# Kernel optimization log

Measured on AMD Instinct MI355X. Metric: run time of the kernel, lower is better.

The kernel has to match this reference:

```python
import jax, jax.numpy as jnp
import numpy as np

B, N, D, H, K = 8, 1024, 1024, 64, 20


def setup_inputs() -> dict:
    key = jax.random.key(0)
    ks = jax.random.split(key, 8)
    s = 0.05
    return {
        "f1": jax.random.normal(ks[0], (B, N, D), jnp.float32),
        "f2": jax.random.normal(ks[1], (B, N, D), jnp.float32),
        "W1a": jax.random.normal(ks[2], (D, H), jnp.float32) * s,
        "b1a": jnp.zeros((H,), jnp.float32),
        "W2a": jax.random.normal(ks[3], (H, H), jnp.float32) * s,
        "b2a": jnp.zeros((H,), jnp.float32),
        "W1b": jax.random.normal(ks[4], (H, H), jnp.float32) * s,
        "b1b": jnp.zeros((H,), jnp.float32),
        "W2b": jax.random.normal(ks[5], (H, H), jnp.float32) * s,
        "b2b": jnp.zeros((H,), jnp.float32),
        "k": K,
    }


def _knn_idx(f, k):
    # f: [N, D] -> indices [N, k] of k nearest neighbors (self excluded)
    sq = jnp.sum(f * f, axis=-1)                      # [N]
    d = sq[:, None] + sq[None, :] - 2.0 * (f @ f.T)   # [N, N] squared dists
    n = f.shape[0]
    d = d + jnp.eye(n, dtype=f.dtype) * jnp.float32(1e10)  # exclude self-loop
    _, idx = jax.lax.top_k(-d, k)                     # smallest distances
    return idx


def _gin_layer(x, idx, W1, b1, W2, b2):
    # GINConv with eps=0: MLP(x + sum_{j in N(i)} x_j)
    agg = jnp.sum(x[idx], axis=1)                     # [N, D] neighbor-sum
    h = x + agg
    h = jnp.maximum(h @ W1 + b1, 0.0) @ W2 + b2
    return h


def reference(f1, f2, W1a, b1a, W2a, b2a, W1b, b1b, W2b, b2b, k):
    def encode(f):
        idx = _knn_idx(f, k)
        h = _gin_layer(f, idx, W1a, b1a, W2a, b2a)
        h = _gin_layer(h, idx, W1b, b1b, W2b, b2b)
        return h

    def per_sample(a, b):
        z1 = encode(a)                                # [N, H]
        z2 = encode(b)                                # [N, H]
        sim = z1 @ z2.T                               # [N, N]
        return jax.nn.softmax(sim, axis=1)

    return jax.vmap(per_sample)(f1, f2)               # [B, N, N]
```

## Files before the change

### kernel.cpp

```cpp
#include <hip/hip_runtime.h>
#include <hip/hip_bf16.h>
#include <math.h>

#define BATCH 8
#define NPTS  1024
#define DIM   1024
#define HID   64
#define KNN   20
#define NMAT  16
#define KPACK 3072

typedef __attribute__((ext_vector_type(8))) short short8;
typedef __attribute__((ext_vector_type(4))) float floatx4;

__device__ __forceinline__ const float* mat_base(const float* f1, const float* f2, int m) {
    return (m < BATCH) ? (f1 + (size_t)m * NPTS * DIM)
                       : (f2 + (size_t)(m - BATCH) * NPTS * DIM);
}

__device__ __forceinline__ unsigned short f2bf_bits(float v) {
    __hip_bfloat16 h = __float2bfloat16(v);
    return *(unsigned short*)&h;
}
__device__ __forceinline__ float bfbits2f(unsigned short b) {
    union { unsigned u; float f; } c; c.u = ((unsigned)b) << 16; return c.f;
}

__global__ __launch_bounds__(256) void split_ymlp_kernel(const float* __restrict__ f1,
                                                         const float* __restrict__ f2,
                                                         const float* __restrict__ W,
                                                         unsigned short* __restrict__ H,
                                                         float* __restrict__ sq,
                                                         float* __restrict__ y) {
    int row0 = blockIdx.x * 64;
    int m = row0 >> 10;
    const float* A = mat_base(f1, f2, m) + (size_t)(row0 & (NPTS - 1)) * DIM;
    unsigned short* Hb = H + (size_t)row0 * KPACK;
    __shared__ float As[64][20];
    __shared__ float Ws[16][HID];
    int tid = threadIdx.x;
    int r = tid >> 2, cq = (tid & 3) * 4;
    int ty = tid >> 4, tx = tid & 15;
    float acc[4][4];
    #pragma unroll
    for (int i = 0; i < 4; ++i)
        #pragma unroll
        for (int j = 0; j < 4; ++j) acc[i][j] = 0.f;
    float sqp = 0.f;
    unsigned short* Hr = Hb + (size_t)r * KPACK + cq;

    for (int kk = 0; kk < DIM; kk += 16) {
        float4 a = *(const float4*)&A[(size_t)r * DIM + kk + cq];
        {
            float vv[4] = {a.x, a.y, a.z, a.w};
            unsigned short h1[4], h2[4], h3[4];
            #pragma unroll
            for (int c = 0; c < 4; ++c) {
                unsigned short b1 = f2bf_bits(vv[c]);
                float r1 = vv[c] - bfbits2f(b1);
                unsigned short b2 = f2bf_bits(r1);
                float r2 = r1 - bfbits2f(b2);
                unsigned short b3 = f2bf_bits(r2);
                h1[c] = b1; h2[c] = b2; h3[c] = b3;
            }
            *(ushort4*)&Hr[kk]        = *(ushort4*)&h1[0];
            *(ushort4*)&Hr[1024 + kk] = *(ushort4*)&h2[0];
            *(ushort4*)&Hr[2048 + kk] = *(ushort4*)&h3[0];
            sqp += a.x * a.x + a.y * a.y + a.z * a.z + a.w * a.w;
        }
        *(float4*)&As[r][cq] = a;
        {
            int d = tid >> 4, hh = (tid & 15) * 4;
            *(float4*)&Ws[d][hh] = *(const float4*)&W[(size_t)(kk + d) * HID + hh];
        }
        __syncthreads();
        #pragma unroll
        for (int k = 0; k < 16; ++k) {
            float av[4];
            #pragma unroll
            for (int ii = 0; ii < 4; ++ii) av[ii] = As[ty * 4 + ii][k];
            float4 w = *(const float4*)&Ws[k][tx * 4];
            #pragma unroll
            for (int ii = 0; ii < 4; ++ii) {
                acc[ii][0] += av[ii] * w.x;
                acc[ii][1] += av[ii] * w.y;
                acc[ii][2] += av[ii] * w.z;
                acc[ii][3] += av[ii] * w.w;
            }
        }
        __syncthreads();
    }
    sqp += __shfl_down(sqp, 1);
    sqp += __shfl_down(sqp, 2);
    if ((tid & 3) == 0) sq[row0 + r] = sqp;
    #pragma unroll
    for (int ii = 0; ii < 4; ++ii)
        *(float4*)&y[(size_t)(row0 + ty * 4 + ii) * HID + tx * 4] = *(float4*)&acc[ii][0];
}

__global__ __launch_bounds__(256) void gram_mfma_kernel(const unsigned short* __restrict__ H,
                                                        const float* __restrict__ sq,
                                                        float* __restrict__ dist) {
    int bid = blockIdx.x;
    int xcd = bid & 7;
    int g = bid >> 3;
    int m = xcd + 8 * (g & 1);
    int t = g >> 1;
    int bi = 0;
    { int a = t; while (a >= 8 - bi) { a -= 8 - bi; ++bi; } t = a; }
    int bj = bi + t;
    int ti = bi << 7, tj = bj << 7;

    const unsigned short* Hm = H + (size_t)m * NPTS * KPACK;

    __shared__ __align__(16) unsigned short Asl[24 * 512];
    __shared__ __align__(16) unsigned short Bsl[24 * 512];

    int tid = threadIdx.x;
    int w = tid >> 6, lane = tid & 63;
    int wi = w >> 1, wj = w & 1;
    int r16 = lane & 15, kc = lane >> 4;

    floatx4 acc[4][4];
    #pragma unroll
    for (int a = 0; a < 4; ++a)
        #pragma unroll
        for (int b = 0; b < 4; ++b) acc[a][b] = (floatx4)0.f;

    for (int kk = 0; kk < 1024; kk += 32) {
        __syncthreads();
        #pragma unroll
        for (int c = 0; c < 6; ++c) {
            int ca = w * 6 + c;
            int seg = ca >> 3;
            int rb  = ca & 7;
            size_t koff = (size_t)(seg << 10) + kk + kc * 8;
            const unsigned short* ga = Hm + (size_t)(ti + rb * 16 + r16) * KPACK + koff;
            const unsigned short* gb = Hm + (size_t)(tj + rb * 16 + r16) * KPACK + koff;
            __builtin_amdgcn_global_load_lds(
                (const __attribute__((address_space(1))) void*)ga,
                (__attribute__((address_space(3))) void*)&Asl[ca * 512], 16, 0, 0);
            __builtin_amdgcn_global_load_lds(
                (const __attribute__((address_space(1))) void*)gb,
                (__attribute__((address_space(3))) void*)&Bsl[ca * 512], 16, 0, 0);
        }
        __syncthreads();
        short8 af[3][4];
        #pragma unroll
        for (int s = 0; s < 3; ++s)
            #pragma unroll
            for (int a = 0; a < 4; ++a)
                af[s][a] = *(const short8*)&Asl[(s * 8 + wi * 4 + a) * 512 + lane * 8];
        #pragma unroll
        for (int sb = 0; sb < 3; ++sb) {
            short8 bf[4];
            #pragma unroll
            for (int b = 0; b < 4; ++b)
                bf[b] = *(const short8*)&Bsl[(sb * 8 + wj * 4 + b) * 512 + lane * 8];
            #pragma unroll
            for (int sa = 0; sa < 3; ++sa) {
                if (sa + sb > 2) continue;
                #pragma unroll
                for (int a = 0; a < 4; ++a)
                    #pragma unroll
                    for (int b = 0; b < 4; ++b)
                        acc[a][b] = __builtin_amdgcn_mfma_f32_16x16x32_bf16(af[sa][a], bf[b], acc[a][b], 0, 0, 0);
            }
        }
    }

    const float* sqm = sq + m * NPTS;
    #pragma unroll
    for (int a = 0; a < 4; ++a) {
        int i0 = ti + wi * 64 + a * 16 + (lane >> 4) * 4;
        #pragma unroll
        for (int b = 0; b < 4; ++b) {
            int j = tj + wj * 64 + b * 16 + (lane & 15);
            float sqj = sqm[j];
            #pragma unroll
            for (int r = 0; r < 4; ++r) {
                int i = i0 + r;
                float v = sqm[i] + sqj - 2.f * acc[a][b][r];
                if (i == j) v += 1e10f;
                dist[((size_t)m * NPTS + i) * NPTS + j] = v;
                if (bi != bj) dist[((size_t)m * NPTS + j) * NPTS + i] = v;
            }
        }
    }
}

__global__ __launch_bounds__(256) void topk_kernel(const float* __restrict__ dist,
                                                   int* __restrict__ knn_idx) {
    int tid = threadIdx.x;
    int wave = tid >> 6, lane = tid & 63;
    int row = blockIdx.x * 4 + wave;
    const float* d = dist + (size_t)row * NPTS;
    float v[16];
    #pragma unroll
    for (int s = 0; s < 16; ++s) v[s] = d[s * 64 + lane];
    int myj = 0;
    for (int sel = 0; sel < KNN; ++sel) {
        float bv = v[0]; int bs = 0;
        #pragma unroll
        for (int s = 1; s < 16; ++s)
            if (v[s] < bv) { bv = v[s]; bs = s; }
        int bj = bs * 64 + lane;
        #pragma unroll
        for (int off = 1; off < 64; off <<= 1) {
            float ov = __shfl_xor(bv, off);
            int   oj = __shfl_xor(bj, off);
            if (ov < bv || (ov == bv && oj < bj)) { bv = ov; bj = oj; }
        }
        if ((bj & 63) == lane) v[bj >> 6] = 3e38f;
        if (lane == sel) myj = bj;
    }
    if (lane < KNN) knn_idx[(size_t)row * KNN + lane] = myj;
}

__global__ __launch_bounds__(256) void t1h1_kernel(const float* __restrict__ y,
                                                   const int* __restrict__ knn_idx,
                                                   const float* __restrict__ W,
                                                   const float* __restrict__ bias1,
                                                   const float* __restrict__ bias2,
                                                   float* __restrict__ h1) {
    int row0 = blockIdx.x * 64;
    int m = row0 >> 10;
    __shared__ int nb[64 * KNN];
    __shared__ float t1s[64][65];
    __shared__ float Ws[64][HID];
    __shared__ float b1s[HID], b2s[HID];
    int tid = threadIdx.x;
    for (int k = tid; k < 64 * KNN; k += 256) nb[k] = knn_idx[(size_t)row0 * KNN + k];
    for (int k = tid; k < 64 * HID; k += 256) Ws[k >> 6][k & 63] = W[k];
    if (tid < HID) { b1s[tid] = bias1[tid]; b2s[tid] = bias2[tid]; }
    __syncthreads();
    {
        int r = tid >> 2, c0 = (tid & 3) * 16;
        const float* yr = y + (size_t)(row0 + r) * HID + c0;
        float4 a[4];
        #pragma unroll
        for (int q = 0; q < 4; ++q) a[q] = *(const float4*)&yr[q * 4];
        const float* ym = y + (size_t)(m << 10) * HID;
        #pragma unroll
        for (int t = 0; t < KNN; ++t) {
            const float* yn = ym + (size_t)nb[r * KNN + t] * HID + c0;
            #pragma unroll
            for (int q = 0; q < 4; ++q) {
                float4 v = *(const float4*)&yn[q * 4];
                a[q].x += v.x; a[q].y += v.y; a[q].z += v.z; a[q].w += v.w;
            }
        }
        #pragma unroll
        for (int q = 0; q < 4; ++q) {
            int c = c0 + q * 4;
            t1s[r][c + 0] = fmaxf(a[q].x + b1s[c + 0], 0.f);
            t1s[r][c + 1] = fmaxf(a[q].y + b1s[c + 1], 0.f);
            t1s[r][c + 2] = fmaxf(a[q].z + b1s[c + 2], 0.f);
            t1s[r][c + 3] = fmaxf(a[q].w + b1s[c + 3], 0.f);
        }
    }
    __syncthreads();
    int ty = tid >> 4, tx = tid & 15;
    float acc[4][4];
    #pragma unroll
    for (int i = 0; i < 4; ++i)
        #pragma unroll
        for (int j = 0; j < 4; ++j) acc[i][j] = 0.f;
    #pragma unroll
    for (int k = 0; k < HID; ++k) {
        float a[4];
        #pragma unroll
        for (int ii = 0; ii < 4; ++ii) a[ii] = t1s[ty * 4 + ii][k];
        float4 w = *(const float4*)&Ws[k][tx * 4];
        #pragma unroll
        for (int ii = 0; ii < 4; ++ii) {
            acc[ii][0] += a[ii] * w.x;
            acc[ii][1] += a[ii] * w.y;
            acc[ii][2] += a[ii] * w.z;
            acc[ii][3] += a[ii] * w.w;
        }
    }
    #pragma unroll
    for (int ii = 0; ii < 4; ++ii) {
        float o[4];
        #pragma unroll
        for (int jj = 0; jj < 4; ++jj) o[jj] = acc[ii][jj] + b2s[tx * 4 + jj];
        *(float4*)&h1[(size_t)(row0 + ty * 4 + ii) * HID + tx * 4] = *(float4*)&o[0];
    }
}

__global__ __launch_bounds__(256) void t2z_kernel(const float* __restrict__ h1,
                                                  const int* __restrict__ knn_idx,
                                                  const float* __restrict__ W1,
                                                  const float* __restrict__ bias1,
                                                  const float* __restrict__ W2,
                                                  const float* __restrict__ bias2,
                                                  float* __restrict__ z) {
    int row0 = blockIdx.x * 64;
    int m = row0 >> 10;
    __shared__ int nb[64 * KNN];
    __shared__ float hs[64][65];
    __shared__ float t2s[64][65];
    __shared__ float Ws[64][HID];
    __shared__ float b1s[HID], b2s[HID];
    int tid = threadIdx.x;
    for (int k = tid; k < 64 * KNN; k += 256) nb[k] = knn_idx[(size_t)row0 * KNN + k];
    for (int k = tid; k < 64 * HID; k += 256) Ws[k >> 6][k & 63] = W1[k];
    if (tid < HID) { b1s[tid] = bias1[tid]; b2s[tid] = bias2[tid]; }
    __syncthreads();
    {
        int r = tid >> 2, c0 = (tid & 3) * 16;
        const float* hr = h1 + (size_t)(row0 + r) * HID + c0;
        float4 a[4];
        #pragma unroll
        for (int q = 0; q < 4; ++q) a[q] = *(const float4*)&hr[q * 4];
        const float* hm = h1 + (size_t)(m << 10) * HID;
        #pragma unroll
        for (int t = 0; t < KNN; ++t) {
            const float* hn = hm + (size_t)nb[r * KNN + t] * HID + c0;
            #pragma unroll
            for (int q = 0; q < 4; ++q) {
                float4 v = *(const float4*)&hn[q * 4];
                a[q].x += v.x; a[q].y += v.y; a[q].z += v.z; a[q].w += v.w;
            }
        }
        #pragma unroll
        for (int q = 0; q < 4; ++q) *(float4*)&hs[r][c0 + q * 4] = a[q];
    }
    __syncthreads();
    int ty = tid >> 4, tx = tid & 15;
    float acc[4][4];
    #pragma unroll
    for (int i = 0; i < 4; ++i)
        #pragma unroll
        for (int j = 0; j < 4; ++j) acc[i][j] = 0.f;
    #pragma unroll
    for (int k = 0; k < HID; ++k) {
        float a[4];
        #pragma unroll
        for (int ii = 0; ii < 4; ++ii) a[ii] = hs[ty * 4 + ii][k];
        float4 w = *(const float4*)&Ws[k][tx * 4];
        #pragma unroll
        for (int ii = 0; ii < 4; ++ii) {
            acc[ii][0] += a[ii] * w.x;
            acc[ii][1] += a[ii] * w.y;
            acc[ii][2] += a[ii] * w.z;
            acc[ii][3] += a[ii] * w.w;
        }
    }
    #pragma unroll
    for (int ii = 0; ii < 4; ++ii)
        #pragma unroll
        for (int jj = 0; jj < 4; ++jj)
            t2s[ty * 4 + ii][tx * 4 + jj] = fmaxf(acc[ii][jj] + b1s[tx * 4 + jj], 0.f);
    __syncthreads();
    for (int k = tid; k < 64 * HID; k += 256) Ws[k >> 6][k & 63] = W2[k];
    __syncthreads();
    #pragma unroll
    for (int i = 0; i < 4; ++i)
        #pragma unroll
        for (int j = 0; j < 4; ++j) acc[i][j] = 0.f;
    #pragma unroll
    for (int k = 0; k < HID; ++k) {
        float a[4];
        #pragma unroll
        for (int ii = 0; ii < 4; ++ii) a[ii] = t2s[ty * 4 + ii][k];
        float4 w = *(const float4*)&Ws[k][tx * 4];
        #pragma unroll
        for (int ii = 0; ii < 4; ++ii) {
            acc[ii][0] += a[ii] * w.x;
            acc[ii][1] += a[ii] * w.y;
            acc[ii][2] += a[ii] * w.z;
            acc[ii][3] += a[ii] * w.w;
        }
    }
    #pragma unroll
    for (int ii = 0; ii < 4; ++ii) {
        float o[4];
        #pragma unroll
        for (int jj = 0; jj < 4; ++jj) o[jj] = acc[ii][jj] + b2s[tx * 4 + jj];
        *(float4*)&z[(size_t)(row0 + ty * 4 + ii) * HID + tx * 4] = *(float4*)&o[0];
    }
}

__global__ __launch_bounds__(256) void sim_kernel(const float* __restrict__ z,
                                                  float* __restrict__ logits) {
    int bid = blockIdx.x;
    int b = bid >> 8;
    int tile = bid & 255;
    int ti = (tile >> 4) << 6;
    int tj = (tile & 15) << 6;
    const float* z1 = z + (size_t)b * NPTS * HID;
    const float* z2 = z + (size_t)(BATCH + b) * NPTS * HID;
    __shared__ float Z1[64][68];
    __shared__ float Z2[64][68];
    int tid = threadIdx.x;
    #pragma unroll
    for (int i = 0; i < 4; ++i) {
        int l = tid + i * 256;
        int r = l >> 4, c = (l & 15) * 4;
        *(float4*)&Z1[r][c] = *(const float4*)&z1[(size_t)(ti + r) * HID + c];
        *(float4*)&Z2[r][c] = *(const float4*)&z2[(size_t)(tj + r) * HID + c];
    }
    __syncthreads();
    int ty = tid >> 4, tx = tid & 15;
    float acc[4][4];
    #pragma unroll
    for (int i = 0; i < 4; ++i)
        #pragma unroll
        for (int j = 0; j < 4; ++j) acc[i][j] = 0.f;
    #pragma unroll
    for (int h = 0; h < HID; ++h) {
        float a[4], bb[4];
        #pragma unroll
        for (int ii = 0; ii < 4; ++ii) { a[ii] = Z1[ty * 4 + ii][h]; bb[ii] = Z2[tx * 4 + ii][h]; }
        #pragma unroll
        for (int ii = 0; ii < 4; ++ii)
            #pragma unroll
            for (int jj = 0; jj < 4; ++jj)
                acc[ii][jj] += a[ii] * bb[jj];
    }
    #pragma unroll
    for (int ii = 0; ii < 4; ++ii) {
        float* dst = logits + ((size_t)b * NPTS + ti + ty * 4 + ii) * NPTS + tj + tx * 4;
        *(float4*)&dst[0] = *(float4*)&acc[ii][0];
    }
}

__global__ __launch_bounds__(256) void softmax_kernel(const float* __restrict__ logits,
                                                      float* __restrict__ out) {
    int row = blockIdx.x;
    const float* L = logits + (size_t)row * NPTS;
    __shared__ float buf[NPTS];
    __shared__ float red[8];
    int tid = threadIdx.x;
    int wave = tid >> 6, lane = tid & 63;
    float mx = -3e38f;
    #pragma unroll
    for (int s = 0; s < 4; ++s) {
        float v = L[tid + s * 256];
        buf[tid + s * 256] = v;
        mx = fmaxf(mx, v);
    }
    #pragma unroll
    for (int off = 32; off > 0; off >>= 1) mx = fmaxf(mx, __shfl_down(mx, off));
    if (lane == 0) red[wave] = mx;
    __syncthreads();
    mx = fmaxf(fmaxf(red[0], red[1]), fmaxf(red[2], red[3]));
    float sum = 0.f;
    #pragma unroll
    for (int s = 0; s < 4; ++s) {
        float e = expf(buf[tid + s * 256] - mx);
        buf[tid + s * 256] = e;
        sum += e;
    }
    #pragma unroll
    for (int off = 32; off > 0; off >>= 1) sum += __shfl_down(sum, off);
    if (lane == 0) red[4 + wave] = sum;
    __syncthreads();
    float inv = 1.f / (red[4] + red[5] + red[6] + red[7]);
    #pragma unroll
    for (int s = 0; s < 4; ++s)
        out[(size_t)row * NPTS + tid + s * 256] = buf[tid + s * 256] * inv;
}

extern "C" void kernel_launch(void* const* d_in, const int* in_sizes, int n_in,
                              void* d_out, int out_size, void* d_ws, size_t ws_size,
                              hipStream_t stream) {
    const float* f1  = (const float*)d_in[0];
    const float* f2  = (const float*)d_in[1];
    const float* W1a = (const float*)d_in[2];
    const float* b1a = (const float*)d_in[3];
    const float* W2a = (const float*)d_in[4];
    const float* b2a = (const float*)d_in[5];
    const float* W1b = (const float*)d_in[6];
    const float* b1b = (const float*)d_in[7];
    const float* W2b = (const float*)d_in[8];
    const float* b2b = (const float*)d_in[9];
    float* out = (float*)d_out;

    char* ws = (char*)d_ws;
    unsigned short* H = (unsigned short*)ws;
    float* dist = (float*)(ws + (size_t)NMAT * NPTS * KPACK * sizeof(unsigned short));
    float* sq   = dist + (size_t)NMAT * NPTS * NPTS;
    int*   kidx = (int*)(sq + NMAT * NPTS);
    float* ybuf = (float*)(kidx + NMAT * NPTS * KNN);
    float* h1b  = ybuf + (size_t)NMAT * NPTS * HID;
    float* zb   = h1b + (size_t)NMAT * NPTS * HID;

    split_ymlp_kernel<<<NMAT * NPTS / 64, 256, 0, stream>>>(f1, f2, W1a, H, sq, ybuf);
    gram_mfma_kernel<<<NMAT * 36, 256, 0, stream>>>(H, sq, dist);
    topk_kernel<<<NMAT * NPTS / 4, 256, 0, stream>>>(dist, kidx);
    t1h1_kernel<<<NMAT * NPTS / 64, 256, 0, stream>>>(ybuf, kidx, W2a, b1a, b2a, h1b);
    t2z_kernel<<<NMAT * NPTS / 64, 256, 0, stream>>>(h1b, kidx, W1b, b1b, W2b, b2b, zb);
    sim_kernel<<<BATCH * 256, 256, 0, stream>>>(zb, dist);
    softmax_kernel<<<BATCH * NPTS, 256, 0, stream>>>(dist, out);
}
```

Baseline: 540.2 us.

## Double-buffer gram kernel B tiles and load A fragments directly to registers

Restructures the gram MFMA kernel's K loop into a software pipeline. The B tile is double-buffered in LDS using async global-to-LDS loads, and the A fragments are loaded straight from global memory into a pair of alternating register sets, prefetching the next step while the MFMAs for the current one run. Hand-placed s_waitcnt vmcnt counts and raw barriers replace the __syncthreads pairs, which also removes the LDS round trip for A. This relies on the vmcnt(18) count matching the number of outstanding loads, and the launch_bounds occupancy hint of 2 plus the extra register buffers may raise register pressure.

```diff
diff --git a/kernel.cpp b/kernel.cpp
--- a/kernel.cpp
+++ b/kernel.cpp
@@ -98,9 +98,55 @@
         *(float4*)&y[(size_t)(row0 + ty * 4 + ii) * HID + tx * 4] = *(float4*)&acc[ii][0];
 }
 
-__global__ __launch_bounds__(256) void gram_mfma_kernel(const unsigned short* __restrict__ H,
-                                                        const float* __restrict__ sq,
-                                                        float* __restrict__ dist) {
+#define GRAM_STEP(CUR, NXT, BUF, T)                                                        \
+  {                                                                                        \
+    if ((T) < 31) {                                                                        \
+      int kn = ((T) + 1) * 32;                                                             \
+      _Pragma("unroll")                                                                    \
+      for (int s = 0; s < 3; ++s)                                                          \
+        _Pragma("unroll")                                                                  \
+        for (int a = 0; a < 4; ++a)                                                        \
+          NXT[s][a] = *(const short8*)&Hm[(size_t)(ti + ((wi << 2) + a) * 16 + r16) * KPACK \
+                                          + (size_t)(s << 10) + kn + (kc << 3)];           \
+      _Pragma("unroll")                                                                    \
+      for (int c = 0; c < 6; ++c) {                                                        \
+        int ca = w * 6 + c; int seg = ca >> 3; int rb = ca & 7;                            \
+        const unsigned short* gb = Hm + (size_t)(tj + rb * 16 + r16) * KPACK               \
+                                      + (size_t)(seg << 10) + kn + (kc << 3);              \
+        __builtin_amdgcn_global_load_lds(                                                  \
+            (const __attribute__((address_space(1))) void*)gb,                             \
+            (__attribute__((address_space(3))) void*)&Bsl[(BUF) ^ 1][ca * 512], 16, 0, 0); \
+      }                                                                                    \
+      asm volatile("s_waitcnt vmcnt(18)" ::: "memory");                                    \
+    } else {                                                                               \
+      asm volatile("s_waitcnt vmcnt(0)" ::: "memory");                                     \
+    }                                                                                      \
+    __builtin_amdgcn_s_barrier();                                                          \
+    asm volatile("" ::: "memory");                                                         \
+    _Pragma("unroll")                                                                      \
+    for (int sb = 0; sb < 3; ++sb) {                                                       \
+      short8 bf[4];                                                                        \
+      _Pragma("unroll")                                                                    \
+      for (int b = 0; b < 4; ++b)                                                          \
+        bf[b] = *(const short8*)&Bsl[BUF][(sb * 8 + (wj << 2) + b) * 512 + lane * 8];      \
+      _Pragma("unroll")                                                                    \
+      for (int sa = 0; sa < 3; ++sa) {                                                     \
+        if (sa + sb > 2) continue;                                                         \
+        _Pragma("unroll")                                                                  \
+        for (int a = 0; a < 4; ++a)                                                        \
+          _Pragma("unroll")                                                                \
+          for (int b = 0; b < 4; ++b)                                                      \
+            acc[a][b] = __builtin_amdgcn_mfma_f32_16x16x32_bf16(CUR[sa][a], bf[b],         \
+                                                                acc[a][b], 0, 0, 0);       \
+      }                                                                                    \
+    }                                                                                      \
+    asm volatile("" ::: "memory");                                                         \
+    __builtin_amdgcn_s_barrier();                                                          \
+  }
+
+__global__ __launch_bounds__(256, 2) void gram_mfma_kernel(const unsigned short* __restrict__ H,
+                                                           const float* __restrict__ sq,
+                                                           float* __restrict__ dist) {
     int bid = blockIdx.x;
     int xcd = bid & 7;
     int g = bid >> 3;
@@ -113,8 +159,7 @@
 
     const unsigned short* Hm = H + (size_t)m * NPTS * KPACK;
 
-    __shared__ __align__(16) unsigned short Asl[24 * 512];
-    __shared__ __align__(16) unsigned short Bsl[24 * 512];
+    __shared__ __align__(16) unsigned short Bsl[2][24 * 512];
 
     int tid = threadIdx.x;
     int w = tid >> 6, lane = tid & 63;
@@ -127,46 +172,28 @@
         #pragma unroll
         for (int b = 0; b < 4; ++b) acc[a][b] = (floatx4)0.f;
 
-    for (int kk = 0; kk < 1024; kk += 32) {
-        __syncthreads();
-        #pragma unroll
-        for (int c = 0; c < 6; ++c) {
-            int ca = w * 6 + c;
-            int seg = ca >> 3;
-            int rb  = ca & 7;
-            size_t koff = (size_t)(seg << 10) + kk + kc * 8;
-            const unsigned short* ga = Hm + (size_t)(ti + rb * 16 + r16) * KPACK + koff;
-            const unsigned short* gb = Hm + (size_t)(tj + rb * 16 + r16) * KPACK + koff;
-            __builtin_amdgcn_global_load_lds(
-                (const __attribute__((address_space(1))) void*)ga,
-                (__attribute__((address_space(3))) void*)&Asl[ca * 512], 16, 0, 0);
-            __builtin_amdgcn_global_load_lds(
-                (const __attribute__((address_space(1))) void*)gb,
-                (__attribute__((address_space(3))) void*)&Bsl[ca * 512], 16, 0, 0);
-        }
-        __syncthreads();
-        short8 af[3][4];
-        #pragma unroll
-        for (int s = 0; s < 3; ++s)
-            #pragma unroll
-            for (int a = 0; a < 4; ++a)
-                af[s][a] = *(const short8*)&Asl[(s * 8 + wi * 4 + a) * 512 + lane * 8];
-        #pragma unroll
-        for (int sb = 0; sb < 3; ++sb) {
-            short8 bf[4];
-            #pragma unroll
-            for (int b = 0; b < 4; ++b)
-                bf[b] = *(const short8*)&Bsl[(sb * 8 + wj * 4 + b) * 512 + lane * 8];
-            #pragma unroll
-            for (int sa = 0; sa < 3; ++sa) {
-                if (sa + sb > 2) continue;
-                #pragma unroll
-                for (int a = 0; a < 4; ++a)
-                    #pragma unroll
-                    for (int b = 0; b < 4; ++b)
-                        acc[a][b] = __builtin_amdgcn_mfma_f32_16x16x32_bf16(af[sa][a], bf[b], acc[a][b], 0, 0, 0);
-            }
-        }
+    short8 afA[3][4], afB[3][4];
+
+    #pragma unroll
+    for (int s = 0; s < 3; ++s)
+        #pragma unroll
+        for (int a = 0; a < 4; ++a)
+            afA[s][a] = *(const short8*)&Hm[(size_t)(ti + ((wi << 2) + a) * 16 + r16) * KPACK
+                                            + (size_t)(s << 10) + (kc << 3)];
+    #pragma unroll
+    for (int c = 0; c < 6; ++c) {
+        int ca = w * 6 + c; int seg = ca >> 3; int rb = ca & 7;
+        const unsigned short* gb = Hm + (size_t)(tj + rb * 16 + r16) * KPACK
+                                      + (size_t)(seg << 10) + (kc << 3);
+        __builtin_amdgcn_global_load_lds(
+            (const __attribute__((address_space(1))) void*)gb,
+            (__attribute__((address_space(3))) void*)&Bsl[0][ca * 512], 16, 0, 0);
+    }
+
+    #pragma unroll 1
+    for (int t2 = 0; t2 < 32; t2 += 2) {
+        GRAM_STEP(afA, afB, 0, t2);
+        GRAM_STEP(afB, afA, 1, t2 + 1);
     }
 
     const float* sqm = sq + m * NPTS;
```

Result: slower. 578.9 us (+7.2%).
